# Optimization experiments

Measured on AMD Instinct MI355X. Metric: run time of the kernel, lower is better.

The kernel has to match this reference:

```python
import jax, jax.numpy as jnp
import numpy as np

B, N, F = 4, 1024, 256
AVG_DEG = 16.0


def setup_inputs() -> dict:
    key = jax.random.key(0)
    k1, k2, k3, k4 = jax.random.split(key, 4)
    u = jax.random.uniform(k1, (B, N, N))
    A = (u < AVG_DEG / N).astype(jnp.float32)
    A = jnp.maximum(A, jnp.swapaxes(A, 1, 2))            # symmetric
    A = A * (1.0 - jnp.eye(N, dtype=jnp.float32))        # no self loops (added in forward)
    x = jax.random.normal(k2, (B, N, F), dtype=jnp.float32)
    pos = jax.random.normal(k3, (B, N, 3), dtype=jnp.float32)
    order = jax.random.uniform(k4, (B, N), dtype=jnp.float32)  # 'random' ordering priorities
    node_mask = jnp.ones((B, N), dtype=bool)
    return {"x": x, "adj": A, "pos": pos, "order": order, "node_mask": node_mask}


def _select(order, excluded, included, node_mask):
    # Greedy frontier-based node selection (K-MIS with stride=2).
    Bn, Nn = order.shape
    ar = jnp.arange(Nn)
    idx0 = jnp.argmin(order, axis=-1).astype(jnp.int32)           # [B]
    available = node_mask
    frontier = ar[None, :] == idx0[:, None]                        # scatter idx0 -> True
    selected = jnp.zeros_like(available)

    def cond(st):
        av, fr, sel, idx = st
        return av.any()

    def body(st):
        av, fr, sel, idx = st
        current = ar[None, :] == idx[:, None]                      # [B,N] one-hot
        sel = sel | current
        exc_row = jnp.take_along_axis(excluded, idx[:, None, None], axis=1)[:, 0]  # excluded[current]
        inc_row = jnp.take_along_axis(included, idx[:, None, None], axis=1)[:, 0]  # included[current]
        av = av & ~current & ~exc_row
        fr = (fr | inc_row | ~fr.any(-1, keepdims=True)) & av      # restart frontier if empty
        mo = jnp.where(fr, order, jnp.inf)
        midx = jnp.argmin(mo, axis=-1).astype(jnp.int32)
        has_fr = fr.any(-1)
        idx = jnp.where(has_fr, midx, idx)
        return (av, fr, sel, idx)

    _, _, selected, _ = jax.lax.while_loop(cond, body, (available, frontier, selected, idx0))
    return selected


def _forward(x, adj, pos, order, node_mask):
    Nn = adj.shape[1]
    eye = jnp.eye(Nn, dtype=adj.dtype)
    adj1 = jnp.where(node_mask[:, :, None], adj + eye, 0.0)        # adj_k[1] = A + I, masked rows
    adj2 = adj1 @ adj                                              # adj_k[2] = (A+I) @ A
    excluded = adj1 != 0                                           # adj_k[stride-1].bool()
    included = adj2 != 0                                           # adj_k[stride].bool()
    selected = _select(jax.lax.stop_gradient(order), excluded, included, node_mask)
    # pad K to N instead of data-dependent num_nodes; mask zeroes the padding
    mask_f, perm = jax.lax.top_k(selected.astype(jnp.float32), Nn)  # [B,K], [B,K]
    adj_kernel = jnp.take_along_axis(adj1, perm[:, None, :], axis=2)  # [B,N,K]
    # add_pool: adj^T @ x, then mask
    x_p = jnp.einsum('bnk,bnf->bkf', adj_kernel, x) * mask_f[..., None]
    # mean_pool for pos: add_pool / column degree
    deg = adj_kernel.sum(axis=1)[..., None]                        # [B,K,1]
    pos_p = jnp.einsum('bnk,bnc->bkc', adj_kernel, pos) / deg * mask_f[..., None]
    # coarsened adjacency: gather cols then rows of adj_k[stride], mask both sides
    a = jnp.take_along_axis(adj2, perm[:, None, :], axis=2)
    a = jnp.take_along_axis(a, perm[:, :, None], axis=1)
    a = a * mask_f[:, None, :] * mask_f[:, :, None]
    return x_p, pos_p, a, mask_f.astype(bool)


def reference(x, adj, pos, order, node_mask):
    return _forward(x, adj, pos, order, node_mask)
```

## Files before the change

### kernel.cpp

```cpp
#include <hip/hip_runtime.h>
#include <hip/hip_bf16.h>

#define BB 4
#define NN 1024
#define FF 256

typedef __hip_bfloat16 bf16;
typedef unsigned long long u64;
typedef unsigned int u32;
typedef unsigned char u8;

__device__ __forceinline__ float b2f(bf16 v) { return __bfloat162float(v); }
__device__ __forceinline__ bf16 f2b(float v) { return __float2bfloat16(v); }

__device__ __forceinline__ float ldf(const void* p, size_t i, int isf32) {
    return isf32 ? ((const float*)p)[i] : b2f(((const bf16*)p)[i]);
}
__device__ __forceinline__ void stf(float* p, size_t i, float v) { p[i] = v; }
__device__ __forceinline__ void stf(bf16* p, size_t i, float v) { p[i] = f2b(v); }

__global__ void probe_kernel(const void* adj, int* flag) {
    const float* p = (const float*)adj;
    int idx = blockIdx.x * 256 + threadIdx.x;
    float v = p[idx];
    int ok = (v == 0.0f) || (v == 1.0f);
    int allok = __syncthreads_and(ok);
    if (threadIdx.x == 0 && !allok) atomicAnd(flag, 0);
}

__global__ __launch_bounds__(512) void sort_kernel(const void* __restrict__ order,
                                                   int* __restrict__ sp2node,
                                                   int* __restrict__ node2sp,
                                                   const int* __restrict__ flag) {
    const int b = blockIdx.x, t = threadIdx.x;
    const int isf32 = (*flag != 0);
    __shared__ u64 keys[NN];
    for (int i = t; i < NN; i += 512) {
        float v = ldf(order, (size_t)b * NN + i, isf32);
        u32 ub = __float_as_uint(v);
        u32 sk = (ub & 0x80000000u) ? ~ub : (ub | 0x80000000u);
        keys[i] = ((u64)sk << 32) | (u32)i;
    }
    __syncthreads();
    for (int k = 2; k <= NN; k <<= 1) {
        for (int j = k >> 1; j > 0; j >>= 1) {
            for (int i = t; i < NN; i += 512) {
                int ixj = i ^ j;
                if (ixj > i) {
                    bool up = (i & k) == 0;
                    u64 a = keys[i], c = keys[ixj];
                    if ((a > c) == up) { keys[i] = c; keys[ixj] = a; }
                }
            }
            __syncthreads();
        }
    }
    for (int i = t; i < NN; i += 512) {
        int n = (int)(keys[i] & 0xFFFFFFFFu);
        sp2node[b * NN + i] = n;
        node2sp[b * NN + n] = i;
    }
}

__global__ void packA_kernel(const void* __restrict__ adj, u64* __restrict__ bitsA,
                             const int* __restrict__ flag) {
    const int r = blockIdx.x, b = blockIdx.y, t = threadIdx.x;
    const int isf32 = (*flag != 0);
    const size_t base = (size_t)b * NN * NN + (size_t)r * NN;
    for (int i = 0; i < 4; i++) {
        int j = i * 256 + t;
        u64 bal = __ballot(ldf(adj, base + j, isf32) != 0.0f);
        if ((t & 63) == 0) bitsA[((size_t)b * NN + r) * 16 + i * 4 + (t >> 6)] = bal;
    }
}

__global__ void inc_pack_kernel(const u64* __restrict__ bitsA,
                                const int* __restrict__ sp2node,
                                const int* __restrict__ node2sp,
                                u32* __restrict__ packed) {
    const int r = blockIdx.x, b = blockIdx.y, t = threadIdx.x;
    __shared__ u64 myrow[16], incw[16];
    __shared__ unsigned short nbr[192];
    __shared__ int s2nT[NN];
    __shared__ int cnt;
    if (t == 0) cnt = 0;
    if (t < 16) myrow[t] = bitsA[((size_t)b * NN + r) * 16 + t];
    __syncthreads();
    for (int i = 0; i < 4; i++) {
        int j = i * 256 + t;
        if ((myrow[j >> 6] >> (j & 63)) & 1) {
            int p = atomicAdd(&cnt, 1);
            if (p < 192) nbr[p] = (unsigned short)j;
        }
        s2nT[(j & 15) * 64 + (j >> 4)] = sp2node[b * NN + j];
    }
    __syncthreads();
    const int c = min(cnt, 192);
    if (t < 16) {
        u64 v = myrow[t];
        for (int n = 0; n < c; n++) v |= bitsA[((size_t)b * NN + nbr[n]) * 16 + t];
        incw[t] = v;
    }
    __syncthreads();
    if (t < 64) {
        const int s = node2sp[b * NN + r];
        u32 e16 = 0, i16 = 0;
        for (int q = 0; q < 16; q++) {
            int jn = s2nT[q * 64 + t];
            u32 eb = (u32)((myrow[jn >> 6] >> (jn & 63)) & 1) | (u32)(jn == r);
            u32 ib = (u32)((incw[jn >> 6] >> (jn & 63)) & 1);
            e16 |= eb << q;
            i16 |= ib << q;
        }
        packed[((size_t)b * NN + s) * 64 + t] = e16 | (i16 << 16);
    }
}

__global__ __launch_bounds__(64) void select_kernel(const u32* __restrict__ packed,
                                                    const int* __restrict__ node2sp,
                                                    int* __restrict__ perm,
                                                    int* __restrict__ kcount) {
    const int b = blockIdx.x, l = threadIdx.x;
    __shared__ u8 selS[NN];
    u32 avail = 0xFFFFu, front = 0u, sel = 0u;
    int cur = 0;
    if (l == 0) front = 1u;

    for (int iter = 0; iter < 2 * NN + 8; ++iter) {
        if (__ballot(avail != 0u) == 0ull) break;
        const bool fr_any = (__ballot(front != 0u) != 0ull);
        if ((cur >> 4) == l) sel |= 1u << (cur & 15);
        u32 p = packed[((size_t)b * NN + cur) * 64 + l];
        avail &= ~(p & 0xFFFFu);
        front = (front | (p >> 16) | (fr_any ? 0u : 0xFFFFu)) & avail;
        u64 fb = __ballot(front != 0u);
        if (fb) {
            int lf = __ffsll(fb) - 1;
            u32 f = __shfl(front, lf);
            cur = lf * 16 + (__ffs(f) - 1);
        }
    }

    for (int q = 0; q < 16; q++) selS[l * 16 + q] = (sel >> q) & 1u;
    __syncthreads();
    u32 nodesel = 0;
    const int* n2s = node2sp + b * NN;
    for (int q = 0; q < 16; q++)
        nodesel |= ((u32)selS[n2s[l * 16 + q]]) << q;

    int cnt_sel = __popc(nodesel);
    int ps = cnt_sel;
    for (int off = 1; off < 64; off <<= 1) {
        int v = __shfl_up(ps, off);
        if (l >= off) ps += v;
    }
    const int K = __shfl(ps, 63);
    int pos = ps - cnt_sel;
    u32 m = nodesel;
    while (m) { int i = __ffs(m) - 1; perm[b * NN + pos++] = l * 16 + i; m &= m - 1; }
    int posu = K + l * 16 - (ps - cnt_sel);
    m = (~nodesel) & 0xFFFFu;
    while (m) { int i = __ffs(m) - 1; perm[b * NN + posu++] = l * 16 + i; m &= m - 1; }
    if (l == 0) kcount[b] = K;
}

template <typename OUT>
__global__ void pool_kernel(const u64* __restrict__ bitsA, const void* __restrict__ x,
                            const void* __restrict__ pos,
                            const int* __restrict__ perm, const int* __restrict__ kcount,
                            OUT* __restrict__ out_x, OUT* __restrict__ out_pos,
                            OUT* __restrict__ out_mask, const int* __restrict__ flag) {
    const int k = blockIdx.x, b = blockIdx.y, t = threadIdx.x;
    const int isf32 = (*flag != 0);
    const int K = kcount[b];
    OUT* ox = out_x + ((size_t)b * NN + k) * FF;
    OUT* op = out_pos + ((size_t)b * NN + k) * 3;
    if (t == 0) stf(out_mask, (size_t)b * NN + k, k < K ? 1.0f : 0.0f);
    if (k >= K) {
        stf(ox, t, 0.0f);
        if (t < 3) stf(op, t, 0.0f);
        return;
    }
    const int r = perm[b * NN + k];
    __shared__ u64 myrow[16];
    __shared__ unsigned short nbr[192];
    __shared__ int cnt;
    if (t == 0) cnt = 0;
    if (t < 16) myrow[t] = bitsA[((size_t)b * NN + r) * 16 + t];
    __syncthreads();
    for (int i = 0; i < 4; i++) {
        int j = i * 256 + t;
        if ((myrow[j >> 6] >> (j & 63)) & 1) {
            int p = atomicAdd(&cnt, 1);
            if (p < 192) nbr[p] = (unsigned short)j;
        }
    }
    __syncthreads();
    const int c = min(cnt, 192);
    const size_t xb = (size_t)b * NN * FF;
    float acc = ldf(x, xb + (size_t)r * FF + t, isf32);
    for (int n = 0; n < c; n++) acc += ldf(x, xb + (size_t)nbr[n] * FF + t, isf32);
    stf(ox, t, acc);
    if (t < 3) {
        const size_t pb = (size_t)b * NN * 3;
        float pa = ldf(pos, pb + r * 3 + t, isf32);
        for (int n = 0; n < c; n++) pa += ldf(pos, pb + nbr[n] * 3 + t, isf32);
        stf(op, t, pa / (float)(c + 1));
    }
}

template <typename OUT>
__global__ void coarse_adj_kernel(const u64* __restrict__ bitsA,
                                  const int* __restrict__ perm, const int* __restrict__ kcount,
                                  OUT* __restrict__ out_a) {
    const int i = blockIdx.x, b = blockIdx.y, t = threadIdx.x;
    const int K = kcount[b];
    OUT* oa = out_a + ((size_t)b * NN + i) * NN;
    if (i >= K) {
        for (int q = 0; q < 4; q++) stf(oa, t + q * 256, 0.0f);
        return;
    }
    __shared__ int p[NN];
    __shared__ u64 myrow[16];
    __shared__ u64 rows[192 * 16];
    __shared__ unsigned short nbr[192];
    __shared__ int cnt;
    const int r = perm[b * NN + i];
    if (t == 0) cnt = 0;
    if (t < 16) myrow[t] = bitsA[((size_t)b * NN + r) * 16 + t];
    for (int q = 0; q < 4; q++) { int j = t + q * 256; p[j] = perm[b * NN + j]; }
    __syncthreads();
    for (int q = 0; q < 4; q++) {
        int j = q * 256 + t;
        if ((myrow[j >> 6] >> (j & 63)) & 1) {
            int pp = atomicAdd(&cnt, 1);
            if (pp < 192) nbr[pp] = (unsigned short)j;
        }
    }
    __syncthreads();
    const int c = min(cnt, 192);
    for (int idx = t; idx < c * 16; idx += 256)
        rows[idx] = bitsA[((size_t)b * NN + nbr[idx >> 4]) * 16 + (idx & 15)];
    __syncthreads();
    for (int q = 0; q < 4; q++) {
        int jj = t + q * 256;
        float v = 0.0f;
        if (jj < K) {
            int pj = p[jj];
            int w = pj >> 6, bp = pj & 63;
            int acc = (int)((myrow[w] >> bp) & 1);
            for (int n = 0; n < c; n++)
                acc += (int)((rows[n * 16 + w] >> bp) & 1);
            v = (float)acc;
        }
        stf(oa, jj, v);
    }
}

extern "C" void kernel_launch(void* const* d_in, const int* in_sizes, int n_in,
                              void* d_out, int out_size, void* d_ws, size_t ws_size,
                              hipStream_t stream) {
    const void* x     = d_in[0];
    const void* adj   = d_in[1];
    const void* pos   = d_in[2];
    const void* order = d_in[3];

    char* ws = (char*)d_ws;
    size_t off = 0;
    u64* bitsA   = (u64*)(ws + off); off += (size_t)BB * NN * 16 * 8;
    u32* packed  = (u32*)(ws + off); off += (size_t)BB * NN * 64 * 4;
    int* sp2node = (int*)(ws + off); off += (size_t)BB * NN * 4;
    int* node2sp = (int*)(ws + off); off += (size_t)BB * NN * 4;
    int* perm    = (int*)(ws + off); off += (size_t)BB * NN * 4;
    int* kcnt    = (int*)(ws + off); off += BB * 4;
    int* flag    = (int*)(ws + off);

    bool outf32 = false;
    size_t osz = 0;
    if (hipMemPtrGetInfo(d_out, &osz) == hipSuccess)
        outf32 = (osz >= 4ull * (size_t)out_size);

    probe_kernel<<<256, 256, 0, stream>>>(adj, flag);
    sort_kernel<<<BB, 512, 0, stream>>>(order, sp2node, node2sp, flag);
    packA_kernel<<<dim3(NN, BB), 256, 0, stream>>>(adj, bitsA, flag);
    inc_pack_kernel<<<dim3(NN, BB), 256, 0, stream>>>(bitsA, sp2node, node2sp, packed);
    select_kernel<<<BB, 64, 0, stream>>>(packed, node2sp, perm, kcnt);

    if (outf32) {
        float* out      = (float*)d_out;
        float* out_x    = out;
        float* out_pos  = out_x + (size_t)BB * NN * FF;
        float* out_a    = out_pos + (size_t)BB * NN * 3;
        float* out_mask = out_a + (size_t)BB * NN * NN;
        pool_kernel<float><<<dim3(NN, BB), 256, 0, stream>>>(bitsA, x, pos, perm, kcnt,
                                                             out_x, out_pos, out_mask, flag);
        coarse_adj_kernel<float><<<dim3(NN, BB), 256, 0, stream>>>(bitsA, perm, kcnt, out_a);
    } else {
        bf16* out      = (bf16*)d_out;
        bf16* out_x    = out;
        bf16* out_pos  = out_x + (size_t)BB * NN * FF;
        bf16* out_a    = out_pos + (size_t)BB * NN * 3;
        bf16* out_mask = out_a + (size_t)BB * NN * NN;
        pool_kernel<bf16><<<dim3(NN, BB), 256, 0, stream>>>(bitsA, x, pos, perm, kcnt,
                                                            out_x, out_pos, out_mask, flag);
        coarse_adj_kernel<bf16><<<dim3(NN, BB), 256, 0, stream>>>(bitsA, perm, kcnt, out_a);
    }
}
```

Measured before the change: 174.8 us.

## Prefetch packed rows into cache in select kernel and use popcount for coarse adjacency

The select kernel now runs 256 threads that first stream the batch's whole packed neighbourhood table through a dummy XOR reduction. This warms the cache so the serial single-wave greedy loop sees cache hits instead of DRAM latency on each step. The frontier-restart test is moved after the update, which saves one ballot per iteration in the common case. The coarse adjacency kernel drops the shared-memory neighbour-row gather and atomics and computes each entry as a bitwise AND plus popcount over 16 words of row bits, which adds more global reads per output element.

```diff
diff --git a/kernel.cpp b/kernel.cpp
--- a/kernel.cpp
+++ b/kernel.cpp
@@ -116,52 +116,70 @@
     }
 }
 
-__global__ __launch_bounds__(64) void select_kernel(const u32* __restrict__ packed,
-                                                    const int* __restrict__ node2sp,
-                                                    int* __restrict__ perm,
-                                                    int* __restrict__ kcount) {
-    const int b = blockIdx.x, l = threadIdx.x;
+__global__ __launch_bounds__(256) void select_kernel(const u32* __restrict__ packed,
+                                                     const int* __restrict__ node2sp,
+                                                     int* __restrict__ perm,
+                                                     int* __restrict__ kcount,
+                                                     int* __restrict__ sink) {
+    const int b = blockIdx.x, t = threadIdx.x;
     __shared__ u8 selS[NN];
-    u32 avail = 0xFFFFu, front = 0u, sel = 0u;
-    int cur = 0;
-    if (l == 0) front = 1u;
-
-    for (int iter = 0; iter < 2 * NN + 8; ++iter) {
-        if (__ballot(avail != 0u) == 0ull) break;
-        const bool fr_any = (__ballot(front != 0u) != 0ull);
-        if ((cur >> 4) == l) sel |= 1u << (cur & 15);
-        u32 p = packed[((size_t)b * NN + cur) * 64 + l];
-        avail &= ~(p & 0xFFFFu);
-        front = (front | (p >> 16) | (fr_any ? 0u : 0xFFFFu)) & avail;
-        u64 fb = __ballot(front != 0u);
-        if (fb) {
-            int lf = __ffsll(fb) - 1;
-            u32 f = __shfl(front, lf);
-            cur = lf * 16 + (__ffs(f) - 1);
-        }
-    }
-
-    for (int q = 0; q < 16; q++) selS[l * 16 + q] = (sel >> q) & 1u;
-    __syncthreads();
-    u32 nodesel = 0;
-    const int* n2s = node2sp + b * NN;
-    for (int q = 0; q < 16; q++)
-        nodesel |= ((u32)selS[n2s[l * 16 + q]]) << q;
-
-    int cnt_sel = __popc(nodesel);
-    int ps = cnt_sel;
-    for (int off = 1; off < 64; off <<= 1) {
-        int v = __shfl_up(ps, off);
-        if (l >= off) ps += v;
-    }
-    const int K = __shfl(ps, 63);
-    int pos = ps - cnt_sel;
-    u32 m = nodesel;
-    while (m) { int i = __ffs(m) - 1; perm[b * NN + pos++] = l * 16 + i; m &= m - 1; }
-    int posu = K + l * 16 - (ps - cnt_sel);
-    m = (~nodesel) & 0xFFFFu;
-    while (m) { int i = __ffs(m) - 1; perm[b * NN + posu++] = l * 16 + i; m &= m - 1; }
-    if (l == 0) kcount[b] = K;
+
+    const uint4* pp = (const uint4*)(packed + (size_t)b * NN * 64);
+    u32 acc = 0;
+    for (int i = t; i < NN * 16; i += 256) {
+        uint4 v = pp[i];
+        acc ^= v.x ^ v.y ^ v.z ^ v.w;
+    }
+    if (acc == 0xDEADBEEFu && t == 77777) atomicAdd(sink, 1);
+    __syncthreads();
+
+    if (t < 64) {
+        const int l = t;
+        u32 avail = 0xFFFFu, front = (l == 0) ? 1u : 0u, sel = 0u;
+        int cur = 0;
+        for (int iter = 0; iter < 2 * NN + 8; ++iter) {
+            if (__ballot(avail != 0u) == 0ull) break;
+            if ((cur >> 4) == l) sel |= 1u << (cur & 15);
+            u32 p = packed[((size_t)b * NN + cur) * 64 + l];
+            avail &= ~(p & 0xFFFFu);
+            front = (front | (p >> 16)) & avail;
+            u64 fb = __ballot(front != 0u);
+            if (!fb) {
+                front = avail;
+                fb = __ballot(front != 0u);
+            }
+            if (fb) {
+                int lf = __ffsll(fb) - 1;
+                u32 f = __shfl(front, lf);
+                cur = lf * 16 + (__ffs(f) - 1);
+            }
+        }
+        for (int q = 0; q < 16; q++) selS[l * 16 + q] = (sel >> q) & 1u;
+    }
+    __syncthreads();
+
+    if (t < 64) {
+        const int l = t;
+        u32 nodesel = 0;
+        const int* n2s = node2sp + b * NN;
+        for (int q = 0; q < 16; q++)
+            nodesel |= ((u32)selS[n2s[l * 16 + q]]) << q;
+
+        int cnt_sel = __popc(nodesel);
+        int ps = cnt_sel;
+        for (int off = 1; off < 64; off <<= 1) {
+            int v = __shfl_up(ps, off);
+            if (l >= off) ps += v;
+        }
+        const int K = __shfl(ps, 63);
+        int pos = ps - cnt_sel;
+        u32 m = nodesel;
+        while (m) { int i = __ffs(m) - 1; perm[b * NN + pos++] = l * 16 + i; m &= m - 1; }
+        int posu = K + l * 16 - (ps - cnt_sel);
+        m = (~nodesel) & 0xFFFFu;
+        while (m) { int i = __ffs(m) - 1; perm[b * NN + posu++] = l * 16 + i; m &= m - 1; }
+        if (l == 0) kcount[b] = K;
+    }
 }
 
 template <typename OUT>
@@ -222,35 +240,20 @@
     }
     __shared__ int p[NN];
     __shared__ u64 myrow[16];
-    __shared__ u64 rows[192 * 16];
-    __shared__ unsigned short nbr[192];
-    __shared__ int cnt;
     const int r = perm[b * NN + i];
-    if (t == 0) cnt = 0;
     if (t < 16) myrow[t] = bitsA[((size_t)b * NN + r) * 16 + t];
     for (int q = 0; q < 4; q++) { int j = t + q * 256; p[j] = perm[b * NN + j]; }
-    __syncthreads();
-    for (int q = 0; q < 4; q++) {
-        int j = q * 256 + t;
-        if ((myrow[j >> 6] >> (j & 63)) & 1) {
-            int pp = atomicAdd(&cnt, 1);
-            if (pp < 192) nbr[pp] = (unsigned short)j;
-        }
-    }
-    __syncthreads();
-    const int c = min(cnt, 192);
-    for (int idx = t; idx < c * 16; idx += 256)
-        rows[idx] = bitsA[((size_t)b * NN + nbr[idx >> 4]) * 16 + (idx & 15)];
     __syncthreads();
     for (int q = 0; q < 4; q++) {
         int jj = t + q * 256;
         float v = 0.0f;
         if (jj < K) {
-            int pj = p[jj];
-            int w = pj >> 6, bp = pj & 63;
-            int acc = (int)((myrow[w] >> bp) & 1);
-            for (int n = 0; n < c; n++)
-                acc += (int)((rows[n * 16 + w] >> bp) & 1);
+            const int pj = p[jj];
+            const u64* rj = bitsA + ((size_t)b * NN + pj) * 16;
+            int acc = (int)((myrow[pj >> 6] >> (pj & 63)) & 1);
+#pragma unroll
+            for (int w = 0; w < 16; w++)
+                acc += __popcll(myrow[w] & rj[w]);
             v = (float)acc;
         }
         stf(oa, jj, v);
@@ -273,7 +276,8 @@
     int* node2sp = (int*)(ws + off); off += (size_t)BB * NN * 4;
     int* perm    = (int*)(ws + off); off += (size_t)BB * NN * 4;
     int* kcnt    = (int*)(ws + off); off += BB * 4;
-    int* flag    = (int*)(ws + off);
+    int* flag    = (int*)(ws + off); off += 4;
+    int* sink    = (int*)(ws + off);
 
     bool outf32 = false;
     size_t osz = 0;
@@ -284,7 +288,7 @@
     sort_kernel<<<BB, 512, 0, stream>>>(order, sp2node, node2sp, flag);
     packA_kernel<<<dim3(NN, BB), 256, 0, stream>>>(adj, bitsA, flag);
     inc_pack_kernel<<<dim3(NN, BB), 256, 0, stream>>>(bitsA, sp2node, node2sp, packed);
-    select_kernel<<<BB, 64, 0, stream>>>(packed, node2sp, perm, kcnt);
+    select_kernel<<<BB, 256, 0, stream>>>(packed, node2sp, perm, kcnt, sink);
 
     if (outf32) {
         float* out      = (float*)d_out;
```

Result: no change. 174.9 us (+0.0%).
